# Performance work log

Hardware: AMD Instinct MI355X
Metric: run time of the kernel (lower is better)

Reference implementation:

```python
import jax, jax.numpy as jnp
import numpy as np

B, C, H, W = 4, 192, 128, 128
EQK, EV, HEADS = 192, 192, 8


def setup_inputs() -> dict:
    key = jax.random.key(0)
    ks = jax.random.split(key, 11)
    s = 0.02
    return {
        "q": jax.random.normal(ks[0], (B, C, H, W), jnp.float32),
        "k": jax.random.normal(ks[1], (B, C, H, W), jnp.float32),
        "v": jax.random.normal(ks[2], (B, C, H, W), jnp.float32),
        "Wq": jax.random.normal(ks[3], (EQK, C), jnp.float32) * s,
        "bq": jax.random.normal(ks[4], (EQK,), jnp.float32) * s,
        "Wk": jax.random.normal(ks[5], (EQK, C), jnp.float32) * s,
        "bk": jax.random.normal(ks[6], (EQK,), jnp.float32) * s,
        "Wv": jax.random.normal(ks[7], (EV, C), jnp.float32) * s,
        "bv": jax.random.normal(ks[8], (EV,), jnp.float32) * s,
        "Wo": jax.random.normal(ks[9], (C, EV), jnp.float32) * s,
        "bo": jax.random.normal(ks[10], (C,), jnp.float32) * s,
    }


def reference(q, k, v, Wq, bq, Wk, bk, Wv, bv, Wo, bo):
    b, c, h, w = q.shape
    n = h * w
    d_qk, d_v = EQK // HEADS, EV // HEADS

    def proj(x, Wt, bt, e):
        # 1x1 conv == per-pixel matmul; flatten spatial dims to n tokens
        return (jnp.einsum('oc,bchw->bohw', Wt, x) + bt[None, :, None, None]).reshape(b, e, n)

    # [b, heads, d, n] head split (embed splits contiguously into H*d, matching torch reshape)
    qh = proj(q, Wq, bq, EQK).reshape(b, HEADS, d_qk, n)
    kh = proj(k, Wk, bk, EQK).reshape(b, HEADS, d_qk, n)
    vh = proj(v, Wv, bv, EV).reshape(b, HEADS, d_v, n)

    qh = jax.nn.softmax(qh, axis=2)  # softmax over feature dim d_qk (torch dim=1 on [bh,d,n])
    kh = jax.nn.softmax(kh, axis=3)  # softmax over token dim n   (torch dim=2 on [bh,d,n])

    # linear attention: context = K @ V^T -> [b, H, d_qk, d_v]; then context^T @ Q
    ctx = jnp.einsum('bhdn,bhen->bhde', kh, vh)
    yh = jnp.einsum('bhde,bhdn->bhen', ctx, qh)  # [b, H, d_v, n]

    y = yh.reshape(b, EV, h, w)
    out = jnp.einsum('oc,bchw->bohw', Wo, y) + bo[None, :, None, None]
    return out
```

## Files before the change

kernel.cpp:

```cpp
#include <hip/hip_runtime.h>

#define CC 192
#define NN 16384
#define QXST 104
#define QST 200

typedef unsigned short u16;
typedef __attribute__((ext_vector_type(4))) float f32x4;
typedef __attribute__((ext_vector_type(8))) __bf16 bf16x8;
typedef __attribute__((ext_vector_type(8))) u16 u16x8;
typedef __attribute__((ext_vector_type(4))) u16 u16x4;

union FragU { u16x8 u; bf16x8 b; };

__device__ __forceinline__ u16 f2bf(float f) {
  union { float f; unsigned u; } x; x.f = f;
  return (u16)((x.u + 0x7FFFu + ((x.u >> 16) & 1u)) >> 16);
}
__device__ __forceinline__ float bf2f(u16 h) {
  union { unsigned u; float f; } x; x.u = ((unsigned)h) << 16;
  return x.f;
}

__device__ __forceinline__ void gemm_stage_compute(
    const float* __restrict__ xb, const u16* __restrict__ Wp,
    int t0, int tid, f32x4 acc[3][4], u16 (*Xs)[QXST])
{
  const int lg = (tid >> 4) & 3, lc = tid & 15;
  const int wave = tid >> 6, e0 = wave * 48;
  const int sn = tid & 63, scg = tid >> 6;
#pragma unroll
  for (int et = 0; et < 3; ++et)
#pragma unroll
    for (int nt = 0; nt < 4; ++nt)
      acc[et][nt] = f32x4{0.f, 0.f, 0.f, 0.f};

#pragma unroll
  for (int hf = 0; hf < 2; ++hf) {
#pragma unroll
    for (int i = 0; i < 6; ++i) {
      int cl = scg * 4 + i * 16;
      const float* src = xb + (size_t)(hf * 96 + cl) * NN + t0 + sn;
      u16x4 p;
      p[0] = f2bf(src[0]);
      p[1] = f2bf(src[NN]);
      p[2] = f2bf(src[2 * NN]);
      p[3] = f2bf(src[3 * NN]);
      *reinterpret_cast<u16x4*>(&Xs[sn][cl]) = p;
    }
    __syncthreads();
#pragma unroll
    for (int ks = 0; ks < 3; ++ks) {
      FragU a[3], bb[4];
#pragma unroll
      for (int et = 0; et < 3; ++et)
        a[et].u = *reinterpret_cast<const u16x8*>(
            &Wp[(e0 + et * 16 + lc) * 192 + hf * 96 + ks * 32 + lg * 8]);
#pragma unroll
      for (int nt = 0; nt < 4; ++nt)
        bb[nt].u = *reinterpret_cast<const u16x8*>(&Xs[nt * 16 + lc][ks * 32 + lg * 8]);
#pragma unroll
      for (int et = 0; et < 3; ++et)
#pragma unroll
        for (int nt = 0; nt < 4; ++nt)
          acc[et][nt] = __builtin_amdgcn_mfma_f32_16x16x32_bf16(a[et].b, bb[nt].b,
                                                               acc[et][nt], 0, 0, 0);
    }
    __syncthreads();
  }
}

__global__ __launch_bounds__(256, 2)
void kproj(const float* __restrict__ k, const float* __restrict__ v,
           const u16* __restrict__ Wb, const float* __restrict__ bk,
           const float* __restrict__ bv, u16* __restrict__ Sexp,
           u16* __restrict__ Vbuf)
{
  __shared__ __align__(16) u16 Xs[64][QXST];
  const int b = blockIdx.y, pj = blockIdx.z;
  const int t0 = blockIdx.x * 64;
  const int tid = threadIdx.x;
  const int lg = (tid >> 4) & 3, lc = tid & 15;
  const int wave = tid >> 6, e0 = wave * 48;

  const float* xb = (pj ? v : k) + (size_t)b * CC * NN;
  const u16* Wp = Wb + (pj ? 2 : 1) * 36864;
  const float* bias = pj ? bv : bk;
  u16* outp = pj ? Vbuf : Sexp;

  f32x4 acc[3][4];
  gemm_stage_compute(xb, Wp, t0, tid, acc, Xs);

#pragma unroll
  for (int et = 0; et < 3; ++et)
#pragma unroll
    for (int r = 0; r < 4; ++r) {
      const int e = e0 + et * 16 + lg * 4 + r;
      const float bb = bias[e];
      u16* orow = outp + (size_t)(b * 192 + e) * NN + t0;
#pragma unroll
      for (int nt = 0; nt < 4; ++nt) {
        float val = acc[et][nt][r] + bb;
        if (!pj) val = __expf(val);
        orow[nt * 16 + lc] = f2bf(val);
      }
    }
}

__global__ __launch_bounds__(512, 2)
void kctx(const u16* __restrict__ Sexp, const u16* __restrict__ Vbuf,
          float* __restrict__ part)
{
  const int b = blockIdx.y, slab = blockIdx.x;
  const int tid = threadIdx.x;
  const int h = tid >> 6;
  const int lg = (tid >> 4) & 3, lc = tid & 15;
  const int n0 = slab * 128;
  const size_t basee = (size_t)b * 192 * NN;

  f32x4 cacc[2][2];
#pragma unroll
  for (int mt = 0; mt < 2; ++mt)
#pragma unroll
    for (int nt = 0; nt < 2; ++nt) cacc[mt][nt] = f32x4{0.f, 0.f, 0.f, 0.f};

#pragma unroll
  for (int ks = 0; ks < 4; ++ks) {
    const int tok = n0 + ks * 32 + lg * 8;
    FragU av[2], bs[2];
#pragma unroll
    for (int mt = 0; mt < 2; ++mt) {
      int row = h * 24 + mt * 16 + lc;
      if (row > 191) row = 191;
      av[mt].u = *reinterpret_cast<const u16x8*>(&Vbuf[basee + (size_t)row * NN + tok]);
      bs[mt].u = *reinterpret_cast<const u16x8*>(&Sexp[basee + (size_t)row * NN + tok]);
    }
#pragma unroll
    for (int mt = 0; mt < 2; ++mt)
#pragma unroll
      for (int nt = 0; nt < 2; ++nt)
        cacc[mt][nt] = __builtin_amdgcn_mfma_f32_16x16x32_bf16(
            av[mt].b, bs[nt].b, cacc[mt][nt], 0, 0, 0);
  }

  float* pp = part + (((size_t)(b * 128 + slab)) * 8 + h) * 576;
#pragma unroll
  for (int mt = 0; mt < 2; ++mt)
#pragma unroll
    for (int nt = 0; nt < 2; ++nt)
#pragma unroll
      for (int r = 0; r < 4; ++r) {
        const int dv = mt * 16 + lg * 4 + r;
        const int d = nt * 16 + lc;
        if (dv < 24 && d < 24) pp[dv * 24 + d] = cacc[mt][nt][r];
      }
}

__global__ __launch_bounds__(256, 2)
void krow(const u16* __restrict__ Sexp, float* __restrict__ ksum)
{
  __shared__ float red[4];
  const int row = blockIdx.x;
  const int tid = threadIdx.x;
  const u16* p = Sexp + (size_t)row * NN;
  float s = 0.f;
#pragma unroll
  for (int i = 0; i < 8; ++i) {
    u16x8 vv = *reinterpret_cast<const u16x8*>(&p[(i * 256 + tid) * 8]);
#pragma unroll
    for (int j = 0; j < 8; ++j) s += bf2f(vv[j]);
  }
#pragma unroll
  for (int off = 1; off < 64; off <<= 1) s += __shfl_xor(s, off);
  if ((tid & 63) == 0) red[tid >> 6] = s;
  __syncthreads();
  if (tid == 0) ksum[row] = red[0] + red[1] + red[2] + red[3];
}

__global__ void kr2(const float* __restrict__ part, const float* __restrict__ ksum,
                    float* __restrict__ ctx)
{
  const int idx = blockIdx.x * 256 + threadIdx.x;
  if (idx >= 4608) return;
  const int b = blockIdx.y;
  const int h = idx / 576, rem = idx % 576;
  const int d = rem % 24;
  float s = 0.f;
  const float* pp = part + (size_t)b * 128 * 4608 + idx;
#pragma unroll 8
  for (int j = 0; j < 128; ++j) s += pp[(size_t)j * 4608];
  ctx[(size_t)b * 4608 + idx] = s / ksum[b * 192 + h * 24 + d];
}

__global__ void km(const float* __restrict__ Wo, const float* __restrict__ ctx,
                   u16* __restrict__ Meff)
{
  const int o = blockIdx.x, b = blockIdx.y, j = threadIdx.x;
  const int h = j / 24, d = j % 24;
  const float* Wrow = Wo + o * 192 + h * 24;
  const float* crow = ctx + (size_t)b * 4608 + h * 576 + d;
  float acc = 0.f;
#pragma unroll
  for (int dv = 0; dv < 24; ++dv) acc += Wrow[dv] * crow[dv * 24];
  Meff[(b * 192 + o) * 192 + j] = f2bf(acc);
}

__global__ __launch_bounds__(256, 2)
void kq(const float* __restrict__ q, const u16* __restrict__ Wb,
        const float* __restrict__ bq, const u16* __restrict__ Meff,
        const float* __restrict__ bo, float* __restrict__ out)
{
  __shared__ __align__(16) u16 Xs[64][QXST];
  __shared__ __align__(16) u16 SsT[64][QST];

  const int b = blockIdx.y;
  const int t0 = blockIdx.x * 64;
  const int tid = threadIdx.x;
  const int lg = (tid >> 4) & 3, lc = tid & 15;
  const int wave = tid >> 6, e0 = wave * 48;
  const u16* Mb = Meff + b * 36864;

  f32x4 acc[3][4];

  gemm_stage_compute(q + (size_t)b * CC * NN, Wb, t0, tid, acc, Xs);
#pragma unroll
  for (int et = 0; et < 3; ++et)
#pragma unroll
    for (int r = 0; r < 4; ++r) {
      int e = e0 + et * 16 + lg * 4 + r;
      float bias = bq[e];
#pragma unroll
      for (int nt = 0; nt < 4; ++nt)
        SsT[nt * 16 + lc][e] = f2bf(acc[et][nt][r] + bias);
    }
  __syncthreads();

#pragma unroll
  for (int ii = 0; ii < 2; ++ii) {
    const int item = ii * 256 + tid;
    const int n = item & 63, h = item >> 6;
    u16* rowp = &SsT[n][h * 24];
    float vals[24];
    float m = -1e30f;
#pragma unroll
    for (int d = 0; d < 24; ++d) {
      vals[d] = bf2f(rowp[d]);
      m = fmaxf(m, vals[d]);
    }
    float s = 0.f;
#pragma unroll
    for (int d = 0; d < 24; ++d) { vals[d] = __expf(vals[d] - m); s += vals[d]; }
    const float inv = 1.f / s;
#pragma unroll
    for (int d = 0; d < 24; ++d) rowp[d] = f2bf(vals[d] * inv);
  }
  __syncthreads();

#pragma unroll
  for (int et = 0; et < 3; ++et)
#pragma unroll
    for (int nt = 0; nt < 4; ++nt) acc[et][nt] = f32x4{0.f, 0.f, 0.f, 0.f};
#pragma unroll
  for (int ks = 0; ks < 6; ++ks) {
    FragU a[3], bb[4];
#pragma unroll
    for (int et = 0; et < 3; ++et)
      a[et].u = *reinterpret_cast<const u16x8*>(
          &Mb[(e0 + et * 16 + lc) * 192 + ks * 32 + lg * 8]);
#pragma unroll
    for (int nt = 0; nt < 4; ++nt)
      bb[nt].u = *reinterpret_cast<const u16x8*>(&SsT[nt * 16 + lc][ks * 32 + lg * 8]);
#pragma unroll
    for (int et = 0; et < 3; ++et)
#pragma unroll
      for (int nt = 0; nt < 4; ++nt)
        acc[et][nt] = __builtin_amdgcn_mfma_f32_16x16x32_bf16(a[et].b, bb[nt].b,
                                                             acc[et][nt], 0, 0, 0);
  }

#pragma unroll
  for (int et = 0; et < 3; ++et)
#pragma unroll
    for (int r = 0; r < 4; ++r) {
      int row = e0 + et * 16 + lg * 4 + r;
      float bias = bo[row];
#pragma unroll
      for (int nt = 0; nt < 4; ++nt)
        out[(size_t)(b * 192 + row) * NN + t0 + nt * 16 + lc] = acc[et][nt][r] + bias;
    }
}

__global__ void kz(const float* __restrict__ Wq, const float* __restrict__ Wk,
                   const float* __restrict__ Wv, u16* __restrict__ Wb)
{
  const int i = blockIdx.x * 256 + threadIdx.x;
  if (i < 110592) {
    const float* src = (i < 36864) ? Wq : (i < 73728) ? Wk : Wv;
    Wb[i] = f2bf(src[i % 36864]);
  }
}

extern "C" void kernel_launch(void* const* d_in, const int* in_sizes, int n_in,
                              void* d_out, int out_size, void* d_ws, size_t ws_size,
                              hipStream_t stream)
{
  const float* q  = (const float*)d_in[0];
  const float* k  = (const float*)d_in[1];
  const float* v  = (const float*)d_in[2];
  const float* Wq = (const float*)d_in[3];
  const float* bq = (const float*)d_in[4];
  const float* Wk = (const float*)d_in[5];
  const float* bk = (const float*)d_in[6];
  const float* Wv = (const float*)d_in[7];
  const float* bv = (const float*)d_in[8];
  const float* Wo = (const float*)d_in[9];
  const float* bo = (const float*)d_in[10];
  float* out = (float*)d_out;

  char* w = (char*)d_ws;
  u16*   Wb   = (u16*)(w);
  u16*   Sexp = (u16*)(w + 221184);
  u16*   Vbuf = (u16*)(w + 25387008);
  float* part = (float*)(w + 50552832);
  float* ksum = (float*)(w + 59990016);
  float* ctx  = (float*)(w + 59993088);
  u16*   Meff = (u16*)(w + 60066816);

  hipLaunchKernelGGL(kz, dim3(432), dim3(256), 0, stream, Wq, Wk, Wv, Wb);
  hipLaunchKernelGGL(kproj, dim3(256, 4, 2), dim3(256), 0, stream,
                     k, v, Wb, bk, bv, Sexp, Vbuf);
  hipLaunchKernelGGL(krow, dim3(768), dim3(256), 0, stream, Sexp, ksum);
  hipLaunchKernelGGL(kctx, dim3(128, 4), dim3(512), 0, stream, Sexp, Vbuf, part);
  hipLaunchKernelGGL(kr2, dim3(18, 4), dim3(256), 0, stream, part, ksum, ctx);
  hipLaunchKernelGGL(km, dim3(192, 4), dim3(192), 0, stream, Wo, ctx, Meff);
  hipLaunchKernelGGL(kq, dim3(256, 4), dim3(256), 0, stream, q, Wb, bq, Meff, bo, out);
}
```

Before: 100.3 us.

## Load full 192-channel input tile in one pass and reuse one LDS buffer

The two-half staging loop of the projection GEMM is replaced with a single pass. Each thread issues all 48 global loads for the full 192-channel tile into registers, then converts them to bf16 and writes them to one larger LDS tile, and the first weight fragments are preloaded before the barrier. This raises memory-level parallelism and removes one barrier pair per half. In kq the same LDS buffer is reused for the q tile and the softmax tile, adding one extra barrier. The cost is more registers, which could reduce occupancy.

```diff
diff --git a/kernel.cpp b/kernel.cpp
--- a/kernel.cpp
+++ b/kernel.cpp
@@ -2,8 +2,7 @@
 
 #define CC 192
 #define NN 16384
-#define QXST 104
-#define QST 200
+#define XST 198
 
 typedef unsigned short u16;
 typedef __attribute__((ext_vector_type(4))) float f32x4;
@@ -22,74 +21,68 @@
   return x.f;
 }
 
-__device__ __forceinline__ void gemm_stage_compute(
-    const float* __restrict__ xb, const u16* __restrict__ Wp,
-    int t0, int tid, f32x4 acc[3][4], u16 (*Xs)[QXST])
-{
-  const int lg = (tid >> 4) & 3, lc = tid & 15;
-  const int wave = tid >> 6, e0 = wave * 48;
-  const int sn = tid & 63, scg = tid >> 6;
-#pragma unroll
-  for (int et = 0; et < 3; ++et)
-#pragma unroll
-    for (int nt = 0; nt < 4; ++nt)
-      acc[et][nt] = f32x4{0.f, 0.f, 0.f, 0.f};
-
-#pragma unroll
-  for (int hf = 0; hf < 2; ++hf) {
-#pragma unroll
-    for (int i = 0; i < 6; ++i) {
-      int cl = scg * 4 + i * 16;
-      const float* src = xb + (size_t)(hf * 96 + cl) * NN + t0 + sn;
-      u16x4 p;
-      p[0] = f2bf(src[0]);
-      p[1] = f2bf(src[NN]);
-      p[2] = f2bf(src[2 * NN]);
-      p[3] = f2bf(src[3 * NN]);
-      *reinterpret_cast<u16x4*>(&Xs[sn][cl]) = p;
-    }
-    __syncthreads();
-#pragma unroll
-    for (int ks = 0; ks < 3; ++ks) {
-      FragU a[3], bb[4];
-#pragma unroll
-      for (int et = 0; et < 3; ++et)
-        a[et].u = *reinterpret_cast<const u16x8*>(
-            &Wp[(e0 + et * 16 + lc) * 192 + hf * 96 + ks * 32 + lg * 8]);
-#pragma unroll
-      for (int nt = 0; nt < 4; ++nt)
-        bb[nt].u = *reinterpret_cast<const u16x8*>(&Xs[nt * 16 + lc][ks * 32 + lg * 8]);
-#pragma unroll
-      for (int et = 0; et < 3; ++et)
-#pragma unroll
-        for (int nt = 0; nt < 4; ++nt)
-          acc[et][nt] = __builtin_amdgcn_mfma_f32_16x16x32_bf16(a[et].b, bb[nt].b,
-                                                               acc[et][nt], 0, 0, 0);
-    }
-    __syncthreads();
-  }
-}
-
 __global__ __launch_bounds__(256, 2)
 void kproj(const float* __restrict__ k, const float* __restrict__ v,
            const u16* __restrict__ Wb, const float* __restrict__ bk,
            const float* __restrict__ bv, u16* __restrict__ Sexp,
            u16* __restrict__ Vbuf)
 {
-  __shared__ __align__(16) u16 Xs[64][QXST];
+  __shared__ __align__(16) u16 Xs[64][XST];
   const int b = blockIdx.y, pj = blockIdx.z;
   const int t0 = blockIdx.x * 64;
   const int tid = threadIdx.x;
   const int lg = (tid >> 4) & 3, lc = tid & 15;
   const int wave = tid >> 6, e0 = wave * 48;
+  const int sn = tid & 63;
 
   const float* xb = (pj ? v : k) + (size_t)b * CC * NN;
   const u16* Wp = Wb + (pj ? 2 : 1) * 36864;
   const float* bias = pj ? bv : bk;
   u16* outp = pj ? Vbuf : Sexp;
 
+  f32x4 p[12];
+#pragma unroll
+  for (int i = 0; i < 12; ++i) {
+    const float* src = xb + (size_t)(wave * 4 + i * 16) * NN + t0 + sn;
+    p[i][0] = src[0]; p[i][1] = src[NN]; p[i][2] = src[2 * NN]; p[i][3] = src[3 * NN];
+  }
+#pragma unroll
+  for (int i = 0; i < 12; ++i) {
+    u16x4 pk;
+    pk[0] = f2bf(p[i][0]); pk[1] = f2bf(p[i][1]);
+    pk[2] = f2bf(p[i][2]); pk[3] = f2bf(p[i][3]);
+    *reinterpret_cast<u16x4*>(&Xs[sn][wave * 4 + i * 16]) = pk;
+  }
+
+  FragU a0[3];
+#pragma unroll
+  for (int et = 0; et < 3; ++et)
+    a0[et].u = *reinterpret_cast<const u16x8*>(&Wp[(e0 + et * 16 + lc) * 192 + lg * 8]);
+
+  __syncthreads();
+
   f32x4 acc[3][4];
-  gemm_stage_compute(xb, Wp, t0, tid, acc, Xs);
+#pragma unroll
+  for (int et = 0; et < 3; ++et)
+#pragma unroll
+    for (int nt = 0; nt < 4; ++nt) acc[et][nt] = f32x4{0.f, 0.f, 0.f, 0.f};
+
+#pragma unroll
+  for (int ks = 0; ks < 6; ++ks) {
+    FragU a[3], bb[4];
+#pragma unroll
+    for (int et = 0; et < 3; ++et)
+      a[et] = (ks == 0) ? a0[et] : *(FragU*)&Wp[(e0 + et * 16 + lc) * 192 + ks * 32 + lg * 8];
+#pragma unroll
+    for (int nt = 0; nt < 4; ++nt)
+      bb[nt].u = *reinterpret_cast<const u16x8*>(&Xs[nt * 16 + lc][ks * 32 + lg * 8]);
+#pragma unroll
+    for (int et = 0; et < 3; ++et)
+#pragma unroll
+      for (int nt = 0; nt < 4; ++nt)
+        acc[et][nt] = __builtin_amdgcn_mfma_f32_16x16x32_bf16(a[et].b, bb[nt].b,
+                                                             acc[et][nt], 0, 0, 0);
+  }
 
 #pragma unroll
   for (int et = 0; et < 3; ++et)
@@ -210,28 +203,68 @@
         const float* __restrict__ bq, const u16* __restrict__ Meff,
         const float* __restrict__ bo, float* __restrict__ out)
 {
-  __shared__ __align__(16) u16 Xs[64][QXST];
-  __shared__ __align__(16) u16 SsT[64][QST];
+  __shared__ __align__(16) u16 S[64][XST];
 
   const int b = blockIdx.y;
   const int t0 = blockIdx.x * 64;
   const int tid = threadIdx.x;
   const int lg = (tid >> 4) & 3, lc = tid & 15;
   const int wave = tid >> 6, e0 = wave * 48;
+  const int sn = tid & 63;
   const u16* Mb = Meff + b * 36864;
 
+  f32x4 p[12];
+  const float* xb = q + (size_t)b * CC * NN;
+#pragma unroll
+  for (int i = 0; i < 12; ++i) {
+    const float* src = xb + (size_t)(wave * 4 + i * 16) * NN + t0 + sn;
+    p[i][0] = src[0]; p[i][1] = src[NN]; p[i][2] = src[2 * NN]; p[i][3] = src[3 * NN];
+  }
+#pragma unroll
+  for (int i = 0; i < 12; ++i) {
+    u16x4 pk;
+    pk[0] = f2bf(p[i][0]); pk[1] = f2bf(p[i][1]);
+    pk[2] = f2bf(p[i][2]); pk[3] = f2bf(p[i][3]);
+    *reinterpret_cast<u16x4*>(&S[sn][wave * 4 + i * 16]) = pk;
+  }
+  FragU a0[3];
+#pragma unroll
+  for (int et = 0; et < 3; ++et)
+    a0[et].u = *reinterpret_cast<const u16x8*>(&Wb[(e0 + et * 16 + lc) * 192 + lg * 8]);
+  __syncthreads();
+
   f32x4 acc[3][4];
-
-  gemm_stage_compute(q + (size_t)b * CC * NN, Wb, t0, tid, acc, Xs);
+#pragma unroll
+  for (int et = 0; et < 3; ++et)
+#pragma unroll
+    for (int nt = 0; nt < 4; ++nt) acc[et][nt] = f32x4{0.f, 0.f, 0.f, 0.f};
+#pragma unroll
+  for (int ks = 0; ks < 6; ++ks) {
+    FragU a[3], bb[4];
+#pragma unroll
+    for (int et = 0; et < 3; ++et)
+      a[et] = (ks == 0) ? a0[et] : *(FragU*)&Wb[(e0 + et * 16 + lc) * 192 + ks * 32 + lg * 8];
+#pragma unroll
+    for (int nt = 0; nt < 4; ++nt)
+      bb[nt].u = *reinterpret_cast<const u16x8*>(&S[nt * 16 + lc][ks * 32 + lg * 8]);
+#pragma unroll
+    for (int et = 0; et < 3; ++et)
+#pragma unroll
+      for (int nt = 0; nt < 4; ++nt)
+        acc[et][nt] = __builtin_amdgcn_mfma_f32_16x16x32_bf16(a[et].b, bb[nt].b,
+                                                             acc[et][nt], 0, 0, 0);
+  }
+  __syncthreads();
+
 #pragma unroll
   for (int et = 0; et < 3; ++et)
 #pragma unroll
     for (int r = 0; r < 4; ++r) {
-      int e = e0 + et * 16 + lg * 4 + r;
-      float bias = bq[e];
-#pragma unroll
-      for (int nt = 0; nt < 4; ++nt)
-        SsT[nt * 16 + lc][e] = f2bf(acc[et][nt][r] + bias);
+      const int e = e0 + et * 16 + lg * 4 + r;
+      const float bias = bq[e];
+#pragma unroll
+      for (int nt = 0; nt < 4; ++nt)
+        S[nt * 16 + lc][e] = f2bf(acc[et][nt][r] + bias);
     }
   __syncthreads();
 
@@ -239,7 +272,7 @@
   for (int ii = 0; ii < 2; ++ii) {
     const int item = ii * 256 + tid;
     const int n = item & 63, h = item >> 6;
-    u16* rowp = &SsT[n][h * 24];
+    u16* rowp = &S[n][h * 24];
     float vals[24];
     float m = -1e30f;
 #pragma unroll
@@ -269,7 +302,7 @@
           &Mb[(e0 + et * 16 + lc) * 192 + ks * 32 + lg * 8]);
 #pragma unroll
     for (int nt = 0; nt < 4; ++nt)
-      bb[nt].u = *reinterpret_cast<const u16x8*>(&SsT[nt * 16 + lc][ks * 32 + lg * 8]);
+      bb[nt].u = *reinterpret_cast<const u16x8*>(&S[nt * 16 + lc][ks * 32 + lg * 8]);
 #pragma unroll
     for (int et = 0; et < 3; ++et)
 #pragma unroll
@@ -282,8 +315,8 @@
   for (int et = 0; et < 3; ++et)
 #pragma unroll
     for (int r = 0; r < 4; ++r) {
-      int row = e0 + et * 16 + lg * 4 + r;
-      float bias = bo[row];
+      const int row = e0 + et * 16 + lg * 4 + r;
+      const float bias = bo[row];
 #pragma unroll
       for (int nt = 0; nt < 4; ++nt)
         out[(size_t)(b * 192 + row) * NN + t0 + nt * 16 + lc] = acc[et][nt][r] + bias;
```

Result: slower. 107.9 us (+7.6%).

## Pipeline kproj with async global-to-LDS loads and fuse key row-sum

Applied to the files above, without the earlier changes.

Rewrites the K/V projection kernel to use 128-token tiles with 512 threads, streaming fp32 input chunks straight into double-buffered LDS via global_load_lds and prefetching weight fragments, so memory loads overlap the MFMA work. The softmax denominator for keys is now accumulated in the projection epilogue with shuffles and atomicAdd, which removes the separate krow pass that re-read Sexp; ksum is zeroed in kz. kq launch bounds are raised to 4 blocks per CU. The risks are float atomic ordering nondeterminism, extra LDS-side bf16 conversion work, and register pressure from the higher occupancy target.

```diff
diff --git a/kernel.cpp b/kernel.cpp
--- a/kernel.cpp
+++ b/kernel.cpp
@@ -2,6 +2,9 @@
 
 #define CC 192
 #define NN 16384
+#define TKB 128
+#define CHS 32
+#define LSTRIDE 130
 #define QXST 104
 #define QST 200
 
@@ -22,87 +25,114 @@
   return x.f;
 }
 
-__device__ __forceinline__ void gemm_stage_compute(
-    const float* __restrict__ xb, const u16* __restrict__ Wp,
-    int t0, int tid, f32x4 acc[3][4], u16 (*Xs)[QXST])
-{
-  const int lg = (tid >> 4) & 3, lc = tid & 15;
-  const int wave = tid >> 6, e0 = wave * 48;
-  const int sn = tid & 63, scg = tid >> 6;
-#pragma unroll
-  for (int et = 0; et < 3; ++et)
-#pragma unroll
-    for (int nt = 0; nt < 4; ++nt)
-      acc[et][nt] = f32x4{0.f, 0.f, 0.f, 0.f};
-
-#pragma unroll
-  for (int hf = 0; hf < 2; ++hf) {
-#pragma unroll
-    for (int i = 0; i < 6; ++i) {
-      int cl = scg * 4 + i * 16;
-      const float* src = xb + (size_t)(hf * 96 + cl) * NN + t0 + sn;
-      u16x4 p;
-      p[0] = f2bf(src[0]);
-      p[1] = f2bf(src[NN]);
-      p[2] = f2bf(src[2 * NN]);
-      p[3] = f2bf(src[3 * NN]);
-      *reinterpret_cast<u16x4*>(&Xs[sn][cl]) = p;
-    }
-    __syncthreads();
-#pragma unroll
-    for (int ks = 0; ks < 3; ++ks) {
-      FragU a[3], bb[4];
-#pragma unroll
-      for (int et = 0; et < 3; ++et)
-        a[et].u = *reinterpret_cast<const u16x8*>(
-            &Wp[(e0 + et * 16 + lc) * 192 + hf * 96 + ks * 32 + lg * 8]);
-#pragma unroll
-      for (int nt = 0; nt < 4; ++nt)
-        bb[nt].u = *reinterpret_cast<const u16x8*>(&Xs[nt * 16 + lc][ks * 32 + lg * 8]);
-#pragma unroll
-      for (int et = 0; et < 3; ++et)
-#pragma unroll
-        for (int nt = 0; nt < 4; ++nt)
-          acc[et][nt] = __builtin_amdgcn_mfma_f32_16x16x32_bf16(a[et].b, bb[nt].b,
-                                                               acc[et][nt], 0, 0, 0);
-    }
-    __syncthreads();
-  }
-}
-
-__global__ __launch_bounds__(256, 2)
+__device__ __forceinline__ void gl_lds4(const float* g, float* l) {
+  __builtin_amdgcn_global_load_lds(
+      (const __attribute__((address_space(1))) void*)g,
+      (__attribute__((address_space(3))) void*)l, 4, 0, 0);
+}
+
+__device__ __forceinline__ void dma_chunk(const float* __restrict__ xb, int c,
+                                          int wv, int lane, float* buf) {
+#pragma unroll
+  for (int i = 0; i < 8; ++i) {
+    const int chl = wv * 4 + (i >> 1);
+    const int half = i & 1;
+    const float* src = xb + (size_t)(c * CHS + chl) * NN + half * 64 + lane;
+    gl_lds4(src, &buf[chl * LSTRIDE + half * 64]);
+  }
+}
+
+__global__ __launch_bounds__(512, 2)
 void kproj(const float* __restrict__ k, const float* __restrict__ v,
            const u16* __restrict__ Wb, const float* __restrict__ bk,
            const float* __restrict__ bv, u16* __restrict__ Sexp,
-           u16* __restrict__ Vbuf)
-{
-  __shared__ __align__(16) u16 Xs[64][QXST];
+           u16* __restrict__ Vbuf, float* __restrict__ ksum)
+{
+  __shared__ __align__(16) float Xf[2][CHS * LSTRIDE];
+
   const int b = blockIdx.y, pj = blockIdx.z;
-  const int t0 = blockIdx.x * 64;
+  const int t0 = blockIdx.x * TKB;
   const int tid = threadIdx.x;
-  const int lg = (tid >> 4) & 3, lc = tid & 15;
-  const int wave = tid >> 6, e0 = wave * 48;
-
-  const float* xb = (pj ? v : k) + (size_t)b * CC * NN;
+  const int wv = tid >> 6, lane = tid & 63;
+  const int wr = wv >> 1, wc = wv & 1;
+  const int lg = lane >> 4, lc = lane & 15;
+  const int e0 = wr * 48;
+
+  const float* xb = ((pj ? v : k) + (size_t)b * CC * NN) + t0;
   const u16* Wp = Wb + (pj ? 2 : 1) * 36864;
   const float* bias = pj ? bv : bk;
   u16* outp = pj ? Vbuf : Sexp;
 
   f32x4 acc[3][4];
-  gemm_stage_compute(xb, Wp, t0, tid, acc, Xs);
+#pragma unroll
+  for (int et = 0; et < 3; ++et)
+#pragma unroll
+    for (int nt = 0; nt < 4; ++nt) acc[et][nt] = f32x4{0.f, 0.f, 0.f, 0.f};
+
+  FragU w[2][3];
+
+  dma_chunk(xb, 0, wv, lane, Xf[0]);
+#pragma unroll
+  for (int et = 0; et < 3; ++et)
+    w[0][et].u = *reinterpret_cast<const u16x8*>(&Wp[(e0 + et * 16 + lc) * 192 + lg * 8]);
+  dma_chunk(xb, 1, wv, lane, Xf[1]);
+
+#pragma unroll
+  for (int c = 0; c < 6; ++c) {
+    if (c < 5) asm volatile("s_waitcnt vmcnt(8)" ::: "memory");
+    else       asm volatile("s_waitcnt vmcnt(0)" ::: "memory");
+    __builtin_amdgcn_s_barrier();
+
+    const float* buf = Xf[c & 1];
+    FragU bb[4];
+#pragma unroll
+    for (int nt = 0; nt < 4; ++nt) {
+      u16x8 f;
+#pragma unroll
+      for (int j = 0; j < 8; ++j)
+        f[j] = f2bf(buf[(lg * 8 + j) * LSTRIDE + wc * 64 + nt * 16 + lc]);
+      bb[nt].u = f;
+    }
+#pragma unroll
+    for (int et = 0; et < 3; ++et)
+#pragma unroll
+      for (int nt = 0; nt < 4; ++nt)
+        acc[et][nt] = __builtin_amdgcn_mfma_f32_16x16x32_bf16(w[c & 1][et].b, bb[nt].b,
+                                                             acc[et][nt], 0, 0, 0);
+    if (c < 5) {
+#pragma unroll
+      for (int et = 0; et < 3; ++et)
+        w[(c + 1) & 1][et].u = *reinterpret_cast<const u16x8*>(
+            &Wp[(e0 + et * 16 + lc) * 192 + (c + 1) * 32 + lg * 8]);
+    }
+    __builtin_amdgcn_s_barrier();
+    if (c < 4) dma_chunk(xb, c + 2, wv, lane, Xf[c & 1]);
+  }
 
 #pragma unroll
   for (int et = 0; et < 3; ++et)
 #pragma unroll
     for (int r = 0; r < 4; ++r) {
       const int e = e0 + et * 16 + lg * 4 + r;
-      const float bb = bias[e];
-      u16* orow = outp + (size_t)(b * 192 + e) * NN + t0;
-#pragma unroll
-      for (int nt = 0; nt < 4; ++nt) {
-        float val = acc[et][nt][r] + bb;
-        if (!pj) val = __expf(val);
-        orow[nt * 16 + lc] = f2bf(val);
+      const float bbv = bias[e];
+      u16* orow = outp + (size_t)(b * 192 + e) * NN + t0 + wc * 64;
+      if (!pj) {
+        float sum = 0.f;
+#pragma unroll
+        for (int nt = 0; nt < 4; ++nt) {
+          const float val = __expf(acc[et][nt][r] + bbv);
+          orow[nt * 16 + lc] = f2bf(val);
+          sum += val;
+        }
+        sum += __shfl_xor(sum, 1);
+        sum += __shfl_xor(sum, 2);
+        sum += __shfl_xor(sum, 4);
+        sum += __shfl_xor(sum, 8);
+        if (lc == 0) atomicAdd(&ksum[b * 192 + e], sum);
+      } else {
+#pragma unroll
+        for (int nt = 0; nt < 4; ++nt)
+          orow[nt * 16 + lc] = f2bf(acc[et][nt][r] + bbv);
       }
     }
 }
@@ -154,27 +184,6 @@
         const int d = nt * 16 + lc;
         if (dv < 24 && d < 24) pp[dv * 24 + d] = cacc[mt][nt][r];
       }
-}
-
-__global__ __launch_bounds__(256, 2)
-void krow(const u16* __restrict__ Sexp, float* __restrict__ ksum)
-{
-  __shared__ float red[4];
-  const int row = blockIdx.x;
-  const int tid = threadIdx.x;
-  const u16* p = Sexp + (size_t)row * NN;
-  float s = 0.f;
-#pragma unroll
-  for (int i = 0; i < 8; ++i) {
-    u16x8 vv = *reinterpret_cast<const u16x8*>(&p[(i * 256 + tid) * 8]);
-#pragma unroll
-    for (int j = 0; j < 8; ++j) s += bf2f(vv[j]);
-  }
-#pragma unroll
-  for (int off = 1; off < 64; off <<= 1) s += __shfl_xor(s, off);
-  if ((tid & 63) == 0) red[tid >> 6] = s;
-  __syncthreads();
-  if (tid == 0) ksum[row] = red[0] + red[1] + red[2] + red[3];
 }
 
 __global__ void kr2(const float* __restrict__ part, const float* __restrict__ ksum,
@@ -205,7 +214,55 @@
   Meff[(b * 192 + o) * 192 + j] = f2bf(acc);
 }
 
-__global__ __launch_bounds__(256, 2)
+__device__ __forceinline__ void gemm_stage_compute(
+    const float* __restrict__ xb, const u16* __restrict__ Wp,
+    int t0, int tid, f32x4 acc[3][4], u16 (*Xs)[QXST])
+{
+  const int lg = (tid >> 4) & 3, lc = tid & 15;
+  const int wave = tid >> 6, e0 = wave * 48;
+  const int sn = tid & 63, scg = tid >> 6;
+#pragma unroll
+  for (int et = 0; et < 3; ++et)
+#pragma unroll
+    for (int nt = 0; nt < 4; ++nt)
+      acc[et][nt] = f32x4{0.f, 0.f, 0.f, 0.f};
+
+#pragma unroll
+  for (int hf = 0; hf < 2; ++hf) {
+#pragma unroll
+    for (int i = 0; i < 6; ++i) {
+      int cl = scg * 4 + i * 16;
+      const float* src = xb + (size_t)(hf * 96 + cl) * NN + t0 + sn;
+      u16x4 p;
+      p[0] = f2bf(src[0]);
+      p[1] = f2bf(src[NN]);
+      p[2] = f2bf(src[2 * NN]);
+      p[3] = f2bf(src[3 * NN]);
+      *reinterpret_cast<u16x4*>(&Xs[sn][cl]) = p;
+    }
+    __syncthreads();
+#pragma unroll
+    for (int ks = 0; ks < 3; ++ks) {
+      FragU a[3], bb[4];
+#pragma unroll
+      for (int et = 0; et < 3; ++et)
+        a[et].u = *reinterpret_cast<const u16x8*>(
+            &Wp[(e0 + et * 16 + lc) * 192 + hf * 96 + ks * 32 + lg * 8]);
+#pragma unroll
+      for (int nt = 0; nt < 4; ++nt)
+        bb[nt].u = *reinterpret_cast<const u16x8*>(&Xs[nt * 16 + lc][ks * 32 + lg * 8]);
+#pragma unroll
+      for (int et = 0; et < 3; ++et)
+#pragma unroll
+        for (int nt = 0; nt < 4; ++nt)
+          acc[et][nt] = __builtin_amdgcn_mfma_f32_16x16x32_bf16(a[et].b, bb[nt].b,
+                                                               acc[et][nt], 0, 0, 0);
+    }
+    __syncthreads();
+  }
+}
+
+__global__ __launch_bounds__(256, 4)
 void kq(const float* __restrict__ q, const u16* __restrict__ Wb,
         const float* __restrict__ bq, const u16* __restrict__ Meff,
         const float* __restrict__ bo, float* __restrict__ out)
@@ -291,13 +348,15 @@
 }
 
 __global__ void kz(const float* __restrict__ Wq, const float* __restrict__ Wk,
-                   const float* __restrict__ Wv, u16* __restrict__ Wb)
+                   const float* __restrict__ Wv, u16* __restrict__ Wb,
+                   float* __restrict__ ksum)
 {
   const int i = blockIdx.x * 256 + threadIdx.x;
   if (i < 110592) {
     const float* src = (i < 36864) ? Wq : (i < 73728) ? Wk : Wv;
     Wb[i] = f2bf(src[i % 36864]);
   }
+  if (i < 768) ksum[i] = 0.f;
 }
 
 extern "C" void kernel_launch(void* const* d_in, const int* in_sizes, int n_in,
@@ -326,10 +385,9 @@
   float* ctx  = (float*)(w + 59993088);
   u16*   Meff = (u16*)(w + 60066816);
 
-  hipLaunchKernelGGL(kz, dim3(432), dim3(256), 0, stream, Wq, Wk, Wv, Wb);
-  hipLaunchKernelGGL(kproj, dim3(256, 4, 2), dim3(256), 0, stream,
-                     k, v, Wb, bk, bv, Sexp, Vbuf);
-  hipLaunchKernelGGL(krow, dim3(768), dim3(256), 0, stream, Sexp, ksum);
+  hipLaunchKernelGGL(kz, dim3(432), dim3(256), 0, stream, Wq, Wk, Wv, Wb, ksum);
+  hipLaunchKernelGGL(kproj, dim3(128, 4, 2), dim3(512), 0, stream,
+                     k, v, Wb, bk, bv, Sexp, Vbuf, ksum);
   hipLaunchKernelGGL(kctx, dim3(128, 4), dim3(512), 0, stream, Sexp, Vbuf, part);
   hipLaunchKernelGGL(kr2, dim3(18, 4), dim3(256), 0, stream, part, ksum, ctx);
   hipLaunchKernelGGL(km, dim3(192, 4), dim3(192), 0, stream, Wo, ctx, Meff);
```

Measured after the change: 154.7 us. 54.2% more time.
